# Kernel tuning notes

Hardware: AMD Instinct MI355X
Metric: run time of the kernel (lower is better)

## Reference

```python
import jax, jax.numpy as jnp
import numpy as np

B, N, M, D = 8, 512, 64, 128
H = 64  # mlp_hidden_dim


def setup_inputs() -> dict:
    key = jax.random.key(0)
    ks = jax.random.split(key, 10)
    op_emb = jax.random.normal(ks[0], (B, N, D), dtype=jnp.float32)
    machine_emb = jax.random.normal(ks[1], (B, M, D), dtype=jnp.float32)
    edge_emb = jax.random.normal(ks[2], (B, N, M, D), dtype=jnp.float32)
    action_mask = jax.random.randint(ks[3], (B, N, M), 0, 2) > 0
    s1 = 1.0 / np.sqrt(3 * D)
    s2 = 1.0 / np.sqrt(H)
    W1 = jax.random.uniform(ks[4], (3 * D, H), jnp.float32, -s1, s1)
    b1 = jax.random.uniform(ks[5], (H,), jnp.float32, -s1, s1)
    W2 = jax.random.uniform(ks[6], (H, H), jnp.float32, -s2, s2)
    b2 = jax.random.uniform(ks[7], (H,), jnp.float32, -s2, s2)
    W3 = jax.random.uniform(ks[8], (H, 1), jnp.float32, -s2, s2)
    b3 = jax.random.uniform(ks[9], (1,), jnp.float32, -s2, s2)
    return {"op_emb": op_emb, "machine_emb": machine_emb, "edge_emb": edge_emb,
            "action_mask": action_mask,
            "W1": W1, "b1": b1, "W2": W2, "b2": b2, "W3": W3, "b3": b3}


def reference(op_emb, machine_emb, edge_emb, action_mask, W1, b1, W2, b2, W3, b3):
    # Split first linear over the three concat chunks to avoid materializing
    # the (B,N,M,3D) concat tensor (same math as cat -> Linear).
    Wo, Wm, We = W1[:D], W1[D:2 * D], W1[2 * D:]
    h = (jnp.einsum('bnd,dh->bnh', op_emb, Wo)[:, :, None, :]
         + jnp.einsum('bmd,dh->bmh', machine_emb, Wm)[:, None, :, :]
         + jnp.einsum('bnmd,dh->bnmh', edge_emb, We) + b1)  # (B,N,M,H)
    h = jax.nn.relu(h)
    h = jax.nn.relu(h @ W2 + b2)
    scores = (h @ W3 + b3)[..., 0]  # (B,N,M)
    scores = jnp.where(action_mask, scores, -jnp.inf)
    return jax.nn.log_softmax(scores.reshape(B, N * M), axis=-1)
```

## Files before the change

### kernel.cpp

```cpp
#include <hip/hip_runtime.h>
#include <math.h>

#define Bb 8
#define Nn 512
#define Mm 64
#define Dd 128
#define Hh 64
#define NEG_BIG (-1.0e30f)

typedef __bf16 bf16x8 __attribute__((ext_vector_type(8)));
typedef float  f32x4  __attribute__((ext_vector_type(4)));

#define WET_STR 136
#define W2T_STR 72

#define WS_WET   0u
#define WS_W2T   17408u
#define WS_CWS   26624u
#define WS_AOP   157696u
#define WS_SCORE 1206272u

__global__ __launch_bounds__(256) void wprep_kernel(
    const float* __restrict__ W1, const float* __restrict__ W2, char* __restrict__ ws)
{
    __bf16* WeT = (__bf16*)(ws + WS_WET);
    __bf16* W2T = (__bf16*)(ws + WS_W2T);
    int g = blockIdx.x * 256 + threadIdx.x;
    if (g < Dd * Hh) {
        int d = g >> 6, h = g & 63;
        WeT[h * WET_STR + d] = (__bf16)W1[(size_t)(2 * Dd + d) * Hh + h];
    } else {
        int g2 = g - Dd * Hh;
        int i = g2 >> 6, j = g2 & 63;
        W2T[j * W2T_STR + i] = (__bf16)W2[(size_t)i * Hh + j];
    }
}

__global__ __launch_bounds__(64) void proj_kernel(
    const float* __restrict__ op_emb, const float* __restrict__ machine_emb,
    const float* __restrict__ W1, const float* __restrict__ b1, char* __restrict__ ws)
{
    float* Cws = (float*)(ws + WS_CWS);
    float* Aop = (float*)(ws + WS_AOP);
    const int bid = blockIdx.x;
    const int h = threadIdx.x;
    if (bid < Bb * Mm) {
        const float* mg = machine_emb + (size_t)bid * Dd;
        const float* Wm = W1 + (size_t)Dd * Hh;
        float acc = b1[h];
#pragma unroll 8
        for (int d = 0; d < Dd; ++d) acc = fmaf(mg[d], Wm[d * Hh + h], acc);
        Cws[(size_t)bid * Hh + h] = acc;
    } else {
        const int bn = bid - Bb * Mm;
        const float* og = op_emb + (size_t)bn * Dd;
        float acc = 0.f;
#pragma unroll 8
        for (int d = 0; d < Dd; ++d) acc = fmaf(og[d], W1[d * Hh + h], acc);
        Aop[(size_t)bn * Hh + h] = acc;
    }
}

__global__ __launch_bounds__(256, 4) void main_kernel(
    const float* __restrict__ edge_emb, const int* __restrict__ mask,
    const float* __restrict__ b2, const float* __restrict__ W3,
    const float* __restrict__ b3, char* __restrict__ ws)
{
    __shared__ __bf16 sWeT[Hh * WET_STR];
    __shared__ __bf16 sW2T[Hh * W2T_STR];
    __shared__ __bf16 sH1 [Mm * W2T_STR];
    __shared__ float  sAop[Hh];

    const float* Cws = (const float*)(ws + WS_CWS);
    const float* Aop = (const float*)(ws + WS_AOP);
    float* scores    = (float*)(ws + WS_SCORE);

    const int tid  = threadIdx.x;
    const int bn   = blockIdx.x;
    const int b    = bn >> 9;
    const int w    = tid >> 6;
    const int lane = tid & 63;
    const int q    = lane >> 4;
    const int ln   = lane & 15;

    {
        const float4* srcA = (const float4*)(ws + WS_WET);
        float4* dstA = (float4*)sWeT;
        for (int i = tid; i < (Hh * WET_STR) / 8; i += 256) dstA[i] = srcA[i];
        const float4* srcB = (const float4*)(ws + WS_W2T);
        float4* dstB = (float4*)sW2T;
        for (int i = tid; i < (Hh * W2T_STR) / 8; i += 256) dstB[i] = srcB[i];
        if (tid < Hh) sAop[tid] = Aop[(size_t)bn * Hh + tid];
    }

    const float* Eg = edge_emb + (size_t)bn * (Mm * Dd);
    const int mA = w * 16 + ln;
    float4 e0a = *(const float4*)&Eg[mA * Dd + 0 * 32 + q * 8];
    float4 e0b = *(const float4*)&Eg[mA * Dd + 0 * 32 + q * 8 + 4];
    float4 e1a = *(const float4*)&Eg[mA * Dd + 1 * 32 + q * 8];
    float4 e1b = *(const float4*)&Eg[mA * Dd + 1 * 32 + q * 8 + 4];
    float4 e2a = *(const float4*)&Eg[mA * Dd + 2 * 32 + q * 8];
    float4 e2b = *(const float4*)&Eg[mA * Dd + 2 * 32 + q * 8 + 4];
    float4 e3a = *(const float4*)&Eg[mA * Dd + 3 * 32 + q * 8];
    float4 e3b = *(const float4*)&Eg[mA * Dd + 3 * 32 + q * 8 + 4];

    float cv[16];
#pragma unroll
    for (int t = 0; t < 4; ++t)
#pragma unroll
        for (int r = 0; r < 4; ++r)
            cv[t * 4 + r] = Cws[((size_t)b * Mm + w * 16 + q * 4 + r) * Hh + t * 16 + ln];

    bf16x8 afrag[4];
    {
        float4 lo[4] = {e0a, e1a, e2a, e3a};
        float4 hi[4] = {e0b, e1b, e2b, e3b};
#pragma unroll
        for (int ks = 0; ks < 4; ++ks) {
            bf16x8 a;
            a[0] = (__bf16)lo[ks].x; a[1] = (__bf16)lo[ks].y;
            a[2] = (__bf16)lo[ks].z; a[3] = (__bf16)lo[ks].w;
            a[4] = (__bf16)hi[ks].x; a[5] = (__bf16)hi[ks].y;
            a[6] = (__bf16)hi[ks].z; a[7] = (__bf16)hi[ks].w;
            afrag[ks] = a;
        }
    }
    __syncthreads();

    f32x4 acc[4];
#pragma unroll
    for (int t = 0; t < 4; ++t) acc[t] = (f32x4){0.f, 0.f, 0.f, 0.f};
#pragma unroll
    for (int t = 0; t < 4; ++t) {
#pragma unroll
        for (int ks = 0; ks < 4; ++ks) {
            bf16x8 bfr = *(const bf16x8*)&sWeT[(t * 16 + ln) * WET_STR + ks * 32 + q * 8];
            acc[t] = __builtin_amdgcn_mfma_f32_16x16x32_bf16(afrag[ks], bfr, acc[t], 0, 0, 0);
        }
    }

#pragma unroll
    for (int t = 0; t < 4; ++t) {
        float av = sAop[t * 16 + ln];
#pragma unroll
        for (int r = 0; r < 4; ++r) {
            float v = acc[t][r] + av + cv[t * 4 + r];
            v = fmaxf(v, 0.f);
            sH1[(w * 16 + q * 4 + r) * W2T_STR + t * 16 + ln] = (__bf16)v;
        }
    }
    __syncthreads();

    bf16x8 a2[2];
#pragma unroll
    for (int ks = 0; ks < 2; ++ks)
        a2[ks] = *(const bf16x8*)&sH1[(w * 16 + ln) * W2T_STR + ks * 32 + q * 8];
    f32x4 acc2[4];
#pragma unroll
    for (int t = 0; t < 4; ++t) acc2[t] = (f32x4){0.f, 0.f, 0.f, 0.f};
#pragma unroll
    for (int t = 0; t < 4; ++t) {
#pragma unroll
        for (int ks = 0; ks < 2; ++ks) {
            bf16x8 bfr = *(const bf16x8*)&sW2T[(t * 16 + ln) * W2T_STR + ks * 32 + q * 8];
            acc2[t] = __builtin_amdgcn_mfma_f32_16x16x32_bf16(a2[ks], bfr, acc2[t], 0, 0, 0);
        }
    }

    float p[4] = {0.f, 0.f, 0.f, 0.f};
#pragma unroll
    for (int t = 0; t < 4; ++t) {
        float b2v = b2[t * 16 + ln];
        float w3v = W3[t * 16 + ln];
#pragma unroll
        for (int r = 0; r < 4; ++r)
            p[r] += fmaxf(acc2[t][r] + b2v, 0.f) * w3v;
    }
#pragma unroll
    for (int r = 0; r < 4; ++r) {
        p[r] += __shfl_xor(p[r], 1, 64);
        p[r] += __shfl_xor(p[r], 2, 64);
        p[r] += __shfl_xor(p[r], 4, 64);
        p[r] += __shfl_xor(p[r], 8, 64);
    }
    if (ln == 0) {
        const float bias3 = b3[0];
        const size_t base = (size_t)bn * Mm;
#pragma unroll
        for (int r = 0; r < 4; ++r) {
            int m = w * 16 + q * 4 + r;
            scores[base + m] = mask[base + m] ? (p[r] + bias3) : NEG_BIG;
        }
    }
}

__global__ __launch_bounds__(1024) void lsm_kernel(
    const char* __restrict__ ws, float* __restrict__ out)
{
    const float* s = (const float*)(ws + WS_SCORE) + (size_t)blockIdx.x * (Nn * Mm);
    __shared__ float redA[16];
    __shared__ float redB[16];
    const int tid = threadIdx.x;

    float lm = -INFINITY;
    for (int i = tid; i < Nn * Mm; i += 1024) lm = fmaxf(lm, s[i]);
#pragma unroll
    for (int off = 32; off > 0; off >>= 1) lm = fmaxf(lm, __shfl_xor(lm, off, 64));
    if ((tid & 63) == 0) redA[tid >> 6] = lm;
    __syncthreads();
    float gm = redA[0];
#pragma unroll
    for (int k = 1; k < 16; ++k) gm = fmaxf(gm, redA[k]);

    float ls = 0.f;
    for (int i = tid; i < Nn * Mm; i += 1024) ls += expf(s[i] - gm);
#pragma unroll
    for (int off = 32; off > 0; off >>= 1) ls += __shfl_xor(ls, off, 64);
    if ((tid & 63) == 0) redB[tid >> 6] = ls;
    __syncthreads();
    float gs = 0.f;
#pragma unroll
    for (int k = 0; k < 16; ++k) gs += redB[k];

    const float cc = gm + logf(gs);
    for (int i = tid; i < Nn * Mm; i += 1024)
        out[(size_t)blockIdx.x * (Nn * Mm) + i] = s[i] - cc;
}

extern "C" void kernel_launch(void* const* d_in, const int* in_sizes, int n_in,
                              void* d_out, int out_size, void* d_ws, size_t ws_size,
                              hipStream_t stream)
{
    const float* op_emb      = (const float*)d_in[0];
    const float* machine_emb = (const float*)d_in[1];
    const float* edge_emb    = (const float*)d_in[2];
    const int*   mask        = (const int*)  d_in[3];
    const float* W1 = (const float*)d_in[4];
    const float* b1 = (const float*)d_in[5];
    const float* W2 = (const float*)d_in[6];
    const float* b2 = (const float*)d_in[7];
    const float* W3 = (const float*)d_in[8];
    const float* b3 = (const float*)d_in[9];
    char* ws = (char*)d_ws;

    wprep_kernel<<<48, 256, 0, stream>>>(W1, W2, ws);
    proj_kernel<<<Bb * Mm + Bb * Nn, 64, 0, stream>>>(op_emb, machine_emb, W1, b1, ws);
    main_kernel<<<Bb * Nn, 256, 0, stream>>>(edge_emb, mask, b2, W3, b3, ws);
    lsm_kernel<<<Bb, 1024, 0, stream>>>(ws, (float*)d_out);
}
```

Baseline: 245.8 us.

## Process four rows per block with prefetched edge tiles and fragment-swizzled weights

Each main_kernel block now handles four consecutive (b,n) rows instead of one, so the bf16 weight staging into LDS is paid once per four rows. The edge tile, op projection and mask for the next row are register-prefetched while the current row runs its MFMAs. Weights are pre-swizzled in wprep into MFMA fragment order, so LDS fragment reads become contiguous per lane. The intermediate block barrier is dropped because each wave only reads its own H1 rows, and score stores are vectorized. The cost is fewer blocks, higher register pressure (launch bound lowered to 3) and less parallelism if the lsm stage dominates.

```diff
diff --git a/kernel.cpp b/kernel.cpp
--- a/kernel.cpp
+++ b/kernel.cpp
@@ -6,33 +6,41 @@
 #define Mm 64
 #define Dd 128
 #define Hh 64
+#define Gg 4
 #define NEG_BIG (-1.0e30f)
 
 typedef __bf16 bf16x8 __attribute__((ext_vector_type(8)));
 typedef float  f32x4  __attribute__((ext_vector_type(4)));
 
-#define WET_STR 136
-#define W2T_STR 72
-
-#define WS_WET   0u
-#define WS_W2T   17408u
-#define WS_CWS   26624u
-#define WS_AOP   157696u
-#define WS_SCORE 1206272u
+#define WS_WEB   0u
+#define WS_W2B   16384u
+#define WS_CWS   24576u
+#define WS_AOP   155648u
+#define WS_SCORE 1204224u
 
 __global__ __launch_bounds__(256) void wprep_kernel(
     const float* __restrict__ W1, const float* __restrict__ W2, char* __restrict__ ws)
 {
-    __bf16* WeT = (__bf16*)(ws + WS_WET);
-    __bf16* W2T = (__bf16*)(ws + WS_W2T);
-    int g = blockIdx.x * 256 + threadIdx.x;
-    if (g < Dd * Hh) {
-        int d = g >> 6, h = g & 63;
-        WeT[h * WET_STR + d] = (__bf16)W1[(size_t)(2 * Dd + d) * Hh + h];
-    } else {
-        int g2 = g - Dd * Hh;
-        int i = g2 >> 6, j = g2 & 63;
-        W2T[j * W2T_STR + i] = (__bf16)W2[(size_t)i * Hh + j];
+    __bf16* WeB = (__bf16*)(ws + WS_WEB);
+    __bf16* W2B = (__bf16*)(ws + WS_W2B);
+    int idx = blockIdx.x * 256 + threadIdx.x;
+    if (idx < 8192) {
+        int fid = idx >> 9, rem = idx & 511;
+        int lane = rem >> 3, j = rem & 7;
+        int t = fid >> 2, ks = fid & 3;
+        int q = lane >> 4, ln = lane & 15;
+        int d = ks * 32 + q * 8 + j;
+        int h = t * 16 + ln;
+        WeB[idx] = (__bf16)W1[(size_t)(2 * Dd + d) * Hh + h];
+    } else if (idx < 12288) {
+        int i2 = idx - 8192;
+        int fid = i2 >> 9, rem = i2 & 511;
+        int lane = rem >> 3, j = rem & 7;
+        int t = fid >> 1, ks = fid & 1;
+        int q = lane >> 4, ln = lane & 15;
+        int k = ks * 32 + q * 8 + j;
+        int h = t * 16 + ln;
+        W2B[i2] = (__bf16)W2[(size_t)k * Hh + h];
     }
 }
 
@@ -61,48 +69,36 @@
     }
 }
 
-__global__ __launch_bounds__(256, 4) void main_kernel(
+__global__ __launch_bounds__(256, 3) void main_kernel(
     const float* __restrict__ edge_emb, const int* __restrict__ mask,
     const float* __restrict__ b2, const float* __restrict__ W3,
     const float* __restrict__ b3, char* __restrict__ ws)
 {
-    __shared__ __bf16 sWeT[Hh * WET_STR];
-    __shared__ __bf16 sW2T[Hh * W2T_STR];
-    __shared__ __bf16 sH1 [Mm * W2T_STR];
-    __shared__ float  sAop[Hh];
+    __shared__ __bf16 sWeB[8192];
+    __shared__ __bf16 sW2B[4096];
+    __shared__ __bf16 sH1[Mm * 72];
 
     const float* Cws = (const float*)(ws + WS_CWS);
     const float* Aop = (const float*)(ws + WS_AOP);
     float* scores    = (float*)(ws + WS_SCORE);
 
     const int tid  = threadIdx.x;
-    const int bn   = blockIdx.x;
-    const int b    = bn >> 9;
+    const int lane = tid & 63;
     const int w    = tid >> 6;
-    const int lane = tid & 63;
     const int q    = lane >> 4;
     const int ln   = lane & 15;
+    const int bn0  = blockIdx.x * Gg;
+    const int b    = bn0 >> 9;
+    const int mrow = w * 16 + ln;
 
     {
-        const float4* srcA = (const float4*)(ws + WS_WET);
-        float4* dstA = (float4*)sWeT;
-        for (int i = tid; i < (Hh * WET_STR) / 8; i += 256) dstA[i] = srcA[i];
-        const float4* srcB = (const float4*)(ws + WS_W2T);
-        float4* dstB = (float4*)sW2T;
-        for (int i = tid; i < (Hh * W2T_STR) / 8; i += 256) dstB[i] = srcB[i];
-        if (tid < Hh) sAop[tid] = Aop[(size_t)bn * Hh + tid];
-    }
-
-    const float* Eg = edge_emb + (size_t)bn * (Mm * Dd);
-    const int mA = w * 16 + ln;
-    float4 e0a = *(const float4*)&Eg[mA * Dd + 0 * 32 + q * 8];
-    float4 e0b = *(const float4*)&Eg[mA * Dd + 0 * 32 + q * 8 + 4];
-    float4 e1a = *(const float4*)&Eg[mA * Dd + 1 * 32 + q * 8];
-    float4 e1b = *(const float4*)&Eg[mA * Dd + 1 * 32 + q * 8 + 4];
-    float4 e2a = *(const float4*)&Eg[mA * Dd + 2 * 32 + q * 8];
-    float4 e2b = *(const float4*)&Eg[mA * Dd + 2 * 32 + q * 8 + 4];
-    float4 e3a = *(const float4*)&Eg[mA * Dd + 3 * 32 + q * 8];
-    float4 e3b = *(const float4*)&Eg[mA * Dd + 3 * 32 + q * 8 + 4];
+        const float4* s1 = (const float4*)(ws + WS_WEB);
+        float4* d1 = (float4*)sWeB;
+        for (int i = tid; i < 1024; i += 256) d1[i] = s1[i];
+        const float4* s2 = (const float4*)(ws + WS_W2B);
+        float4* d2 = (float4*)sW2B;
+        for (int i = tid; i < 512; i += 256) d2[i] = s2[i];
+    }
 
     float cv[16];
 #pragma unroll
@@ -110,87 +106,118 @@
 #pragma unroll
         for (int r = 0; r < 4; ++r)
             cv[t * 4 + r] = Cws[((size_t)b * Mm + w * 16 + q * 4 + r) * Hh + t * 16 + ln];
-
-    bf16x8 afrag[4];
+    float b2v[4], w3v[4];
+#pragma unroll
+    for (int t = 0; t < 4; ++t) { b2v[t] = b2[t * 16 + ln]; w3v[t] = W3[t * 16 + ln]; }
+    const float bias3 = b3[0];
+
+    float4 raw[8]; float aopv[4]; int4 mk = {0, 0, 0, 0};
     {
-        float4 lo[4] = {e0a, e1a, e2a, e3a};
-        float4 hi[4] = {e0b, e1b, e2b, e3b};
+        const float* Eg = edge_emb + (size_t)bn0 * (Mm * Dd) + mrow * Dd + q * 8;
 #pragma unroll
         for (int ks = 0; ks < 4; ++ks) {
+            raw[2 * ks]     = *(const float4*)&Eg[ks * 32];
+            raw[2 * ks + 1] = *(const float4*)&Eg[ks * 32 + 4];
+        }
+#pragma unroll
+        for (int t = 0; t < 4; ++t) aopv[t] = Aop[(size_t)bn0 * Hh + t * 16 + ln];
+        if (ln == 0) mk = *(const int4*)&mask[(size_t)bn0 * Mm + w * 16 + q * 4];
+    }
+
+    __syncthreads();
+
+#pragma unroll
+    for (int g = 0; g < Gg; ++g) {
+        const int bn = bn0 + g;
+
+        float4 nraw[8] = {};
+        float  naop[4] = {};
+        int4   nmk = {0, 0, 0, 0};
+        if (g + 1 < Gg) {
+            const float* Eg = edge_emb + (size_t)(bn + 1) * (Mm * Dd) + mrow * Dd + q * 8;
+#pragma unroll
+            for (int ks = 0; ks < 4; ++ks) {
+                nraw[2 * ks]     = *(const float4*)&Eg[ks * 32];
+                nraw[2 * ks + 1] = *(const float4*)&Eg[ks * 32 + 4];
+            }
+#pragma unroll
+            for (int t = 0; t < 4; ++t) naop[t] = Aop[(size_t)(bn + 1) * Hh + t * 16 + ln];
+            if (ln == 0) nmk = *(const int4*)&mask[(size_t)(bn + 1) * Mm + w * 16 + q * 4];
+        }
+
+        bf16x8 af[4];
+#pragma unroll
+        for (int ks = 0; ks < 4; ++ks) {
+            float4 lo = raw[2 * ks], hi = raw[2 * ks + 1];
             bf16x8 a;
-            a[0] = (__bf16)lo[ks].x; a[1] = (__bf16)lo[ks].y;
-            a[2] = (__bf16)lo[ks].z; a[3] = (__bf16)lo[ks].w;
-            a[4] = (__bf16)hi[ks].x; a[5] = (__bf16)hi[ks].y;
-            a[6] = (__bf16)hi[ks].z; a[7] = (__bf16)hi[ks].w;
-            afrag[ks] = a;
-        }
-    }
-    __syncthreads();
-
-    f32x4 acc[4];
-#pragma unroll
-    for (int t = 0; t < 4; ++t) acc[t] = (f32x4){0.f, 0.f, 0.f, 0.f};
-#pragma unroll
-    for (int t = 0; t < 4; ++t) {
-#pragma unroll
-        for (int ks = 0; ks < 4; ++ks) {
-            bf16x8 bfr = *(const bf16x8*)&sWeT[(t * 16 + ln) * WET_STR + ks * 32 + q * 8];
-            acc[t] = __builtin_amdgcn_mfma_f32_16x16x32_bf16(afrag[ks], bfr, acc[t], 0, 0, 0);
-        }
-    }
-
-#pragma unroll
-    for (int t = 0; t < 4; ++t) {
-        float av = sAop[t * 16 + ln];
+            a[0] = (__bf16)lo.x; a[1] = (__bf16)lo.y; a[2] = (__bf16)lo.z; a[3] = (__bf16)lo.w;
+            a[4] = (__bf16)hi.x; a[5] = (__bf16)hi.y; a[6] = (__bf16)hi.z; a[7] = (__bf16)hi.w;
+            af[ks] = a;
+        }
+
+        f32x4 acc[4];
+#pragma unroll
+        for (int t = 0; t < 4; ++t) acc[t] = (f32x4){0.f, 0.f, 0.f, 0.f};
+#pragma unroll
+        for (int t = 0; t < 4; ++t)
+#pragma unroll
+            for (int ks = 0; ks < 4; ++ks) {
+                bf16x8 bfr = *(const bf16x8*)&sWeB[((t * 4 + ks) * 64 + lane) * 8];
+                acc[t] = __builtin_amdgcn_mfma_f32_16x16x32_bf16(af[ks], bfr, acc[t], 0, 0, 0);
+            }
+
+#pragma unroll
+        for (int t = 0; t < 4; ++t) {
+            float av = aopv[t];
+#pragma unroll
+            for (int r = 0; r < 4; ++r) {
+                float v = fmaxf(acc[t][r] + av + cv[t * 4 + r], 0.f);
+                sH1[(w * 16 + q * 4 + r) * 72 + t * 16 + ln] = (__bf16)v;
+            }
+        }
+
+        bf16x8 a2[2];
+#pragma unroll
+        for (int ks = 0; ks < 2; ++ks)
+            a2[ks] = *(const bf16x8*)&sH1[(w * 16 + ln) * 72 + ks * 32 + q * 8];
+        f32x4 c2[4];
+#pragma unroll
+        for (int t = 0; t < 4; ++t) c2[t] = (f32x4){0.f, 0.f, 0.f, 0.f};
+#pragma unroll
+        for (int t = 0; t < 4; ++t)
+#pragma unroll
+            for (int ks = 0; ks < 2; ++ks) {
+                bf16x8 bfr = *(const bf16x8*)&sW2B[((t * 2 + ks) * 64 + lane) * 8];
+                c2[t] = __builtin_amdgcn_mfma_f32_16x16x32_bf16(a2[ks], bfr, c2[t], 0, 0, 0);
+            }
+
+        float p[4] = {0.f, 0.f, 0.f, 0.f};
+#pragma unroll
+        for (int t = 0; t < 4; ++t)
+#pragma unroll
+            for (int r = 0; r < 4; ++r)
+                p[r] += fmaxf(c2[t][r] + b2v[t], 0.f) * w3v[t];
 #pragma unroll
         for (int r = 0; r < 4; ++r) {
-            float v = acc[t][r] + av + cv[t * 4 + r];
-            v = fmaxf(v, 0.f);
-            sH1[(w * 16 + q * 4 + r) * W2T_STR + t * 16 + ln] = (__bf16)v;
-        }
-    }
-    __syncthreads();
-
-    bf16x8 a2[2];
-#pragma unroll
-    for (int ks = 0; ks < 2; ++ks)
-        a2[ks] = *(const bf16x8*)&sH1[(w * 16 + ln) * W2T_STR + ks * 32 + q * 8];
-    f32x4 acc2[4];
-#pragma unroll
-    for (int t = 0; t < 4; ++t) acc2[t] = (f32x4){0.f, 0.f, 0.f, 0.f};
-#pragma unroll
-    for (int t = 0; t < 4; ++t) {
-#pragma unroll
-        for (int ks = 0; ks < 2; ++ks) {
-            bf16x8 bfr = *(const bf16x8*)&sW2T[(t * 16 + ln) * W2T_STR + ks * 32 + q * 8];
-            acc2[t] = __builtin_amdgcn_mfma_f32_16x16x32_bf16(a2[ks], bfr, acc2[t], 0, 0, 0);
-        }
-    }
-
-    float p[4] = {0.f, 0.f, 0.f, 0.f};
-#pragma unroll
-    for (int t = 0; t < 4; ++t) {
-        float b2v = b2[t * 16 + ln];
-        float w3v = W3[t * 16 + ln];
-#pragma unroll
-        for (int r = 0; r < 4; ++r)
-            p[r] += fmaxf(acc2[t][r] + b2v, 0.f) * w3v;
-    }
-#pragma unroll
-    for (int r = 0; r < 4; ++r) {
-        p[r] += __shfl_xor(p[r], 1, 64);
-        p[r] += __shfl_xor(p[r], 2, 64);
-        p[r] += __shfl_xor(p[r], 4, 64);
-        p[r] += __shfl_xor(p[r], 8, 64);
-    }
-    if (ln == 0) {
-        const float bias3 = b3[0];
-        const size_t base = (size_t)bn * Mm;
-#pragma unroll
-        for (int r = 0; r < 4; ++r) {
-            int m = w * 16 + q * 4 + r;
-            scores[base + m] = mask[base + m] ? (p[r] + bias3) : NEG_BIG;
-        }
+            p[r] += __shfl_xor(p[r], 1, 64);
+            p[r] += __shfl_xor(p[r], 2, 64);
+            p[r] += __shfl_xor(p[r], 4, 64);
+            p[r] += __shfl_xor(p[r], 8, 64);
+        }
+        if (ln == 0) {
+            float4 o;
+            o.x = mk.x ? (p[0] + bias3) : NEG_BIG;
+            o.y = mk.y ? (p[1] + bias3) : NEG_BIG;
+            o.z = mk.z ? (p[2] + bias3) : NEG_BIG;
+            o.w = mk.w ? (p[3] + bias3) : NEG_BIG;
+            *(float4*)&scores[(size_t)bn * Mm + w * 16 + q * 4] = o;
+        }
+
+#pragma unroll
+        for (int i = 0; i < 8; ++i) raw[i] = nraw[i];
+#pragma unroll
+        for (int t = 0; t < 4; ++t) aopv[t] = naop[t];
+        mk = nmk;
     }
 }
 
@@ -245,6 +272,6 @@
 
     wprep_kernel<<<48, 256, 0, stream>>>(W1, W2, ws);
     proj_kernel<<<Bb * Mm + Bb * Nn, 64, 0, stream>>>(op_emb, machine_emb, W1, b1, ws);
-    main_kernel<<<Bb * Nn, 256, 0, stream>>>(edge_emb, mask, b2, W3, b3, ws);
+    main_kernel<<<(Bb * Nn) / Gg, 256, 0, stream>>>(edge_emb, mask, b2, W3, b3, ws);
     lsm_kernel<<<Bb, 1024, 0, stream>>>(ws, (float*)d_out);
 }
```

After: 244.4 us. Within noise of the previous version (-0.6%).
